# Kernel optimization log

Measured on AMD Instinct MI355X. Metric: run time of the kernel, lower is better.

Reference implementation:

```python
import jax, jax.numpy as jnp
import numpy as np

HEAD_SIZE = 64
N_EMBD = 1024
BLOCK_SIZE = 2048


def setup_inputs() -> dict:
    key = jax.random.key(0)
    ks = jax.random.split(key, 7)
    B, T = 4, 2048
    s = 1.0 / np.sqrt(N_EMBD)
    return {
        "x": jax.random.normal(ks[0], (B, T, N_EMBD), dtype=jnp.float32),
        "Wq": jax.random.normal(ks[1], (N_EMBD, HEAD_SIZE), dtype=jnp.float32) * s,
        "bq": jnp.zeros((HEAD_SIZE,), dtype=jnp.float32),
        "Wk": jax.random.normal(ks[2], (N_EMBD, HEAD_SIZE), dtype=jnp.float32) * s,
        "bk": jnp.zeros((HEAD_SIZE,), dtype=jnp.float32),
        "Wv": jax.random.normal(ks[3], (N_EMBD, HEAD_SIZE), dtype=jnp.float32) * s,
        "bv": jnp.zeros((HEAD_SIZE,), dtype=jnp.float32),
    }


def reference(x, Wq, bq, Wk, bk, Wv, bv):
    # x: [B, T, n_embd]
    B, T, _ = x.shape
    q = x @ Wq + bq  # [B, T, H]
    k = x @ Wk + bk
    v = x @ Wv + bv
    # Faithful to source: divides by head_size**(-0.5) == multiplies by sqrt(head_size)
    scale = jnp.float32(HEAD_SIZE) ** 0.5
    scores = jnp.einsum("bqh,bkh->bqk", q, k) * scale  # [B, T, T]
    causal = jnp.tril(jnp.ones((T, T), dtype=bool))
    scores = jnp.where(causal, scores, -jnp.inf)
    attn = jax.nn.softmax(scores, axis=-1)  # dropout p=0.0 (eval)
    out = jnp.einsum("bqk,bkh->bqh", attn, v)  # [B, T, H]
    return out
```

## Files before the change

### kernel.cpp

```cpp
#include <hip/hip_runtime.h>
#include <math.h>

#define NE 1024
#define HS 64
#define TT 2048
#define QSC 11.541560327111707f

typedef __bf16    v8bf __attribute__((ext_vector_type(8)));
typedef _Float16  v8h  __attribute__((ext_vector_type(8)));
typedef float     v4f  __attribute__((ext_vector_type(4)));

#define MFMA_BF(a, b, c)  __builtin_amdgcn_mfma_f32_16x16x32_bf16((a), (b), (c), 0, 0, 0)
#define MFMA_F16(a, b, c) __builtin_amdgcn_mfma_f32_16x16x32_f16((a), (b), (c), 0, 0, 0)

__device__ __forceinline__ void gl_lds16(const void* g, void* l) {
    __builtin_amdgcn_global_load_lds(
        (const __attribute__((address_space(1))) unsigned int*)g,
        (__attribute__((address_space(3))) unsigned int*)l, 16, 0, 0);
}

#define SYNC_VM(imm) do {                                   \
    __asm__ __volatile__("" ::: "memory");                  \
    __builtin_amdgcn_s_waitcnt(imm);                        \
    __builtin_amdgcn_s_barrier();                           \
    __asm__ __volatile__("" ::: "memory");                  \
} while (0)
#define WAIT_VM4  0x0F74
#define WAIT_VM0  0x0F70

__global__ __launch_bounds__(256) void prep_w(
    const float* __restrict__ Wq, const float* __restrict__ Wk,
    const float* __restrict__ Wv, char* __restrict__ imgW)
{
    __shared__ float t[64][65];
    const int bx = blockIdx.x, by = blockIdx.y;
    const float* W = (by == 0) ? Wq : ((by == 1) ? Wk : Wv);
    const int tid = threadIdx.x;
    const int cc = tid & 63, r4 = tid >> 6;
    #pragma unroll
    for (int p = 0; p < 16; ++p) {
        const int k = p * 4 + r4;
        t[k][cc] = W[(size_t)(bx * 64 + k) * HS + cc];
    }
    __syncthreads();
    #pragma unroll
    for (int e = 0; e < 4; ++e) {
        const int chunk = tid + e * 256;
        const int s2   = chunk >> 9;
        const int rem  = chunk & 511;
        const int ctl  = rem >> 7;
        const int rem2 = rem & 127;
        const int pl   = rem2 >> 6;
        const int rem3 = rem2 & 63;
        const int c    = rem3 >> 2;
        const int p16  = rem3 & 3;
        const int kb   = s2 * 32 + ((p16 ^ (c & 3)) << 3);
        const int ncol = ctl * 16 + c;
        v8bf o;
        #pragma unroll
        for (int j = 0; j < 8; ++j) {
            const float v = t[kb + j][ncol];
            const __bf16 h = (__bf16)v;
            o[j] = pl ? (__bf16)(v - (float)h) : h;
        }
        *(v8bf*)(imgW + (size_t)(bx * 2 + s2) * 24576
                 + (by * 4 + ctl) * 2048 + pl * 1024 + c * 64 + p16 * 16) = o;
    }
}

__global__ __launch_bounds__(256, 2) void proj(
    const float* __restrict__ x, const char* __restrict__ imgW,
    const float* __restrict__ bq, const float* __restrict__ bk,
    const float* __restrict__ bv,
    _Float16* __restrict__ qh, _Float16* __restrict__ ql,
    _Float16* __restrict__ kp, _Float16* __restrict__ vp)
{
    __shared__ __align__(16) char sbuf[3][16384];

    const int tid = threadIdx.x, lane = tid & 63, cg = tid >> 6;
    const int quad = lane >> 4, l16 = lane & 15;
    const int bx = blockIdx.x;
    const int m0 = (bx >> 1) * 32;
    const int h  = bx & 1;

    const int xrow = cg * 8 + (lane >> 3);
    const int xp   = (lane >> 1) & 3;
    const int xh   = lane & 1;
    const float* gx = x + (size_t)(m0 + xrow) * NE
                        + ((xp ^ (xrow & 3)) << 3) + (xh << 2);
    const int xl = cg * 1024 + lane * 16;
    const char* gw = imgW + (size_t)h * 12288 + (size_t)tid * 16;

    v4f acc[3];
    #pragma unroll
    for (int i = 0; i < 3; ++i) acc[i] = (v4f){0.f, 0.f, 0.f, 0.f};

    #define STAGE(ks, xb_)  do {                                          \
        gl_lds16(gx + (ks) * 32, (xb_) + xl);                             \
        const char* gws_ = gw + (size_t)(ks) * 24576;                     \
        _Pragma("unroll")                                                 \
        for (int j_ = 0; j_ < 3; ++j_)                                    \
            gl_lds16(gws_ + j_ * 4096, (xb_) + 4096 + tid * 16 + j_ * 4096); \
    } while (0)

    auto compute = [&](int ks) {
        const char* xb = sbuf[ks % 3];
        const char* wb = xb + 4096;
        const int mt = cg >> 1;
        const int wc = cg & 1;
        const int rl = mt * 16 + l16;
        const int pA = quad ^ (rl & 3);
        const float4 a0 = *(const float4*)(xb + rl * 128 + pA * 32);
        const float4 a1 = *(const float4*)(xb + rl * 128 + pA * 32 + 16);
        const float av[8] = {a0.x, a0.y, a0.z, a0.w, a1.x, a1.y, a1.z, a1.w};
        v8bf ah, al;
        #pragma unroll
        for (int i = 0; i < 8; ++i) {
            const __bf16 hv = (__bf16)av[i];
            ah[i] = hv;
            al[i] = (__bf16)(av[i] - (float)hv);
        }
        const int wo = l16 * 64 + ((quad ^ (l16 & 3)) << 4);
        #pragma unroll
        for (int j = 0; j < 3; ++j) {
            const char* base = wb + (wc * 3 + j) * 2048 + wo;
            const v8bf bh = *(const v8bf*)(base);
            const v8bf bl = *(const v8bf*)(base + 1024);
            acc[j] = MFMA_BF(ah, bh, acc[j]);
            acc[j] = MFMA_BF(ah, bl, acc[j]);
            acc[j] = MFMA_BF(al, bh, acc[j]);
        }
    };

    STAGE(0, sbuf[0]);
    STAGE(1, sbuf[1]);
    for (int ks = 0; ks < 31; ++ks) {
        SYNC_VM(WAIT_VM4);
        if (ks + 2 < 32) STAGE(ks + 2, sbuf[(ks + 2) % 3]);
        compute(ks);
    }
    SYNC_VM(WAIT_VM0);
    compute(31);
    #undef STAGE

    const int mt = cg >> 1, wc = cg & 1;
    #pragma unroll
    for (int j = 0; j < 3; ++j) {
        const int n = h * 96 + wc * 48 + j * 16 + l16;
        const float bias = (n < 64) ? bq[n] : ((n < 128) ? bk[n - 64] : bv[n - 128]);
        #pragma unroll
        for (int reg = 0; reg < 4; ++reg) {
            const int row = m0 + mt * 16 + quad * 4 + reg;
            const float v = acc[j][reg] + bias;
            if (n < 64) {
                const float s = v * QSC;
                const _Float16 hh = (_Float16)s;
                qh[(size_t)row * HS + n] = hh;
                ql[(size_t)row * HS + n] = (_Float16)(s - (float)hh);
            } else if (n < 128) {
                const int b2 = row >> 11, t = row & 2047, hc = n - 64;
                const size_t base = ((size_t)(b2 * 128) + (t >> 4)) * 1024;
                const int off = (hc < 32)
                    ? (hc >> 3) * 128 + (t & 15) * 8 + (hc & 7)
                    : 512 + ((hc - 32) >> 3) * 128 + (t & 15) * 8 + (hc & 7);
                kp[base + off] = (_Float16)v;
            } else {
                const int b2 = row >> 11, t = row & 2047, hc = n - 128;
                const int cj = t >> 6, tp = t & 63, hg = hc >> 4, hr = hc & 15;
                const size_t base = (((size_t)(b2 * 32) + cj) * 4 + hg) * 1024;
                const int off = (tp < 32)
                    ? (tp >> 3) * 128 + hr * 8 + (tp & 7)
                    : 512 + ((tp - 32) >> 3) * 128 + hr * 8 + (tp & 7);
                vp[base + off] = (_Float16)v;
            }
        }
    }
}

__global__ __launch_bounds__(512, 2) void attn(
    const _Float16* __restrict__ qh, const _Float16* __restrict__ ql,
    const _Float16* __restrict__ kp, const _Float16* __restrict__ vp,
    float* __restrict__ out)
{
    __shared__ __align__(16) char smem_raw[69632];
    _Float16* ps = (_Float16*)smem_raw;
    float*    os = (float*)smem_raw;
    __shared__ float sm[8][2][16], sl[8][2][16];

    const int tid = threadIdx.x, lane = tid & 63, w = tid >> 6;
    const int quad = lane >> 4, l16 = lane & 15;
    const int b = blockIdx.x & 3, pair = blockIdx.x >> 2;
    const int q0t[2] = {(127 - pair) * 16, pair * 16};
    const int ntk0 = (q0t[0] + 16 + 63) >> 6;
    const int ntk1 = (q0t[1] + 16 + 63) >> 6;
    const int total = ntk0 + ntk1;

    v8h Qh0[2], Qh1[2], Ql0[2], Ql1[2];
    #pragma unroll
    for (int t = 0; t < 2; ++t) {
        const size_t qrow = ((size_t)b * TT + q0t[t] + l16) * HS;
        Qh0[t] = *(const v8h*)(qh + qrow + quad * 8);
        Qh1[t] = *(const v8h*)(qh + qrow + 32 + quad * 8);
        Ql0[t] = *(const v8h*)(ql + qrow + quad * 8);
        Ql1[t] = *(const v8h*)(ql + qrow + 32 + quad * 8);
    }

    const v8h vones = {(_Float16)1.f, (_Float16)1.f, (_Float16)1.f, (_Float16)1.f,
                       (_Float16)1.f, (_Float16)1.f, (_Float16)1.f, (_Float16)1.f};

    float mr0[4] = {-3e38f, -3e38f, -3e38f, -3e38f};
    float mr1[4] = {-3e38f, -3e38f, -3e38f, -3e38f};
    v4f o0[4], o1[4], l40, l41;
    #pragma unroll
    for (int i = 0; i < 4; ++i) {
        o0[i] = (v4f){0.f, 0.f, 0.f, 0.f};
        o1[i] = (v4f){0.f, 0.f, 0.f, 0.f};
    }
    l40 = (v4f){0.f, 0.f, 0.f, 0.f};
    l41 = (v4f){0.f, 0.f, 0.f, 0.f};

    _Float16* pw = ps + w * (16 * 72);

    auto loadK = [&](int j0, v8h (&Kf)[8]) {
        #pragma unroll
        for (int nt = 0; nt < 4; ++nt) {
            const _Float16* kb = kp + ((size_t)(b * 128) + (j0 >> 4) + nt) * 1024
                                    + lane * 8;
            Kf[nt * 2]     = *(const v8h*)(kb);
            Kf[nt * 2 + 1] = *(const v8h*)(kb + 512);
        }
    };

    auto doChunk = [&](int j0, int q0c, int t, const v8h (&Kf)[8],
                       float (&mrow)[4], v4f (&o)[4], v4f &o4) {
        v8h Vf[8];
        #pragma unroll
        for (int nt = 0; nt < 4; ++nt) {
            const _Float16* vb = vp + (((size_t)(b * 32) + (j0 >> 6)) * 4 + nt) * 1024
                                    + lane * 8;
            Vf[nt * 2]     = *(const v8h*)(vb);
            Vf[nt * 2 + 1] = *(const v8h*)(vb + 512);
        }
        v4f s[4];
        #pragma unroll
        for (int i = 0; i < 4; ++i) s[i] = (v4f){0.f, 0.f, 0.f, 0.f};
        #pragma unroll
        for (int nt = 0; nt < 4; ++nt) {
            s[nt] = MFMA_F16(Qh0[t], Kf[nt * 2],     s[nt]);
            s[nt] = MFMA_F16(Qh1[t], Kf[nt * 2 + 1], s[nt]);
            s[nt] = MFMA_F16(Ql0[t], Kf[nt * 2],     s[nt]);
            s[nt] = MFMA_F16(Ql1[t], Kf[nt * 2 + 1], s[nt]);
        }
        const int irow = q0c + quad * 4;
        float mx[4] = {-3e38f, -3e38f, -3e38f, -3e38f};
        #pragma unroll
        for (int nt = 0; nt < 4; ++nt)
            #pragma unroll
            for (int reg = 0; reg < 4; ++reg) {
                if (j0 + nt * 16 + l16 > irow + reg) s[nt][reg] = -3e38f;
                mx[reg] = fmaxf(mx[reg], s[nt][reg]);
            }
        #pragma unroll
        for (int off = 8; off; off >>= 1)
            #pragma unroll
            for (int reg = 0; reg < 4; ++reg)
                mx[reg] = fmaxf(mx[reg], __shfl_xor(mx[reg], off));
        float al[4];
        #pragma unroll
        for (int reg = 0; reg < 4; ++reg) {
            const float mn = fmaxf(mrow[reg], mx[reg]);
            al[reg] = exp2f(mrow[reg] - mn);
            mrow[reg] = mn;
        }
        #pragma unroll
        for (int nt = 0; nt < 4; ++nt)
            #pragma unroll
            for (int reg = 0; reg < 4; ++reg) {
                const float p = (j0 + nt * 16 + l16 > irow + reg)
                                    ? 0.f : exp2f(s[nt][reg] - mrow[reg]);
                pw[(quad * 4 + reg) * 72 + nt * 16 + l16] = (_Float16)p;
            }
        #pragma unroll
        for (int nt = 0; nt < 4; ++nt)
            #pragma unroll
            for (int reg = 0; reg < 4; ++reg)
                o[nt][reg] *= al[reg];
        #pragma unroll
        for (int reg = 0; reg < 4; ++reg)
            o4[reg] *= al[reg];
        const v8h Pa0 = *(const v8h*)(pw + l16 * 72 + quad * 8);
        const v8h Pa1 = *(const v8h*)(pw + l16 * 72 + 32 + quad * 8);
        #pragma unroll
        for (int nt = 0; nt < 4; ++nt) {
            o[nt] = MFMA_F16(Pa0, Vf[nt * 2],     o[nt]);
            o[nt] = MFMA_F16(Pa1, Vf[nt * 2 + 1], o[nt]);
        }
        o4 = MFMA_F16(Pa0, vones, o4);
        o4 = MFMA_F16(Pa1, vones, o4);
    };

    auto jof = [&](int c) { return (c < ntk0) ? c * 64 : (c - ntk0) * 64; };

    {
        v8h KA[8], KB[8];
        int c = w;
        loadK(jof(c), KA);
        while (true) {
            int cn = c + 8;
            if (cn < total) loadK(jof(cn), KB);
            if (c < ntk0) doChunk(c * 64,          q0t[0], 0, KA, mr0, o0, l40);
            else          doChunk((c - ntk0) * 64, q0t[1], 1, KA, mr1, o1, l41);
            if (cn >= total) break;
            c = cn; cn = c + 8;
            if (cn < total) loadK(jof(cn), KA);
            if (c < ntk0) doChunk(c * 64,          q0t[0], 0, KB, mr0, o0, l40);
            else          doChunk((c - ntk0) * 64, q0t[1], 1, KB, mr1, o1, l41);
            if (cn >= total) break;
            c = cn;
        }
    }

    if (l16 == 0) {
        #pragma unroll
        for (int reg = 0; reg < 4; ++reg) {
            sm[w][0][quad * 4 + reg] = mr0[reg];
            sl[w][0][quad * 4 + reg] = l40[reg];
            sm[w][1][quad * 4 + reg] = mr1[reg];
            sl[w][1][quad * 4 + reg] = l41[reg];
        }
    }
    __syncthreads();

    #pragma unroll
    for (int t = 0; t < 2; ++t) {
        float sc[4];
        #pragma unroll
        for (int reg = 0; reg < 4; ++reg) {
            const int r = quad * 4 + reg;
            float M = sm[0][t][r];
            #pragma unroll
            for (int i = 1; i < 8; ++i) M = fmaxf(M, sm[i][t][r]);
            const float mw = t ? mr1[reg] : mr0[reg];
            sc[reg] = exp2f(mw - M);
        }
        float* ow = os + (size_t)(w * 2 + t) * (16 * 68);
        #pragma unroll
        for (int nt = 0; nt < 4; ++nt)
            #pragma unroll
            for (int reg = 0; reg < 4; ++reg) {
                const v4f& oo = t ? o1[nt] : o0[nt];
                ow[(quad * 4 + reg) * 68 + nt * 16 + l16] = oo[reg] * sc[reg];
            }
    }
    __syncthreads();

    #pragma unroll
    for (int kk = 0; kk < 4; ++kk) {
        const int g = w * 4 + kk;
        const int t = g >> 4, m = g & 15;
        float M = sm[0][t][m];
        #pragma unroll
        for (int i = 1; i < 8; ++i) M = fmaxf(M, sm[i][t][m]);
        float L = 0.f, val = 0.f;
        #pragma unroll
        for (int i = 0; i < 8; ++i) {
            L   += sl[i][t][m] * exp2f(sm[i][t][m] - M);
            val += os[(size_t)(i * 2 + t) * (16 * 68) + m * 68 + lane];
        }
        out[((size_t)b * TT + q0t[t] + m) * HS + lane] = val / L;
    }
}

extern "C" void kernel_launch(void* const* d_in, const int* in_sizes, int n_in,
                              void* d_out, int out_size, void* d_ws, size_t ws_size,
                              hipStream_t stream)
{
    const float* x  = (const float*)d_in[0];
    const float* Wq = (const float*)d_in[1];
    const float* bq = (const float*)d_in[2];
    const float* Wk = (const float*)d_in[3];
    const float* bk = (const float*)d_in[4];
    const float* Wv = (const float*)d_in[5];
    const float* bv = (const float*)d_in[6];
    float* out = (float*)d_out;

    const int rows = in_sizes[0] / NE;
    char* p = (char*)d_ws;
    char* imgW = p;                           p += (size_t)32 * 24576;
    _Float16* qhb = (_Float16*)p;             p += (size_t)rows * HS * 2;
    _Float16* qlb = (_Float16*)p;             p += (size_t)rows * HS * 2;
    _Float16* kpb = (_Float16*)p;             p += (size_t)rows * HS * 2;
    _Float16* vpb = (_Float16*)p;             p += (size_t)rows * HS * 2;

    prep_w<<<dim3(16, 3), 256, 0, stream>>>(Wq, Wk, Wv, imgW);
    proj<<<rows / 16, 256, 0, stream>>>(x, imgW, bq, bk, bv,
                                        qhb, qlb, kpb, vpb);
    attn<<<rows / 32, 512, 0, stream>>>(qhb, qlb, kpb, vpb, out);
}
```

Measured before the change: 122.1 us.

## Assign one 16-row query tile per block instead of paired causal tiles

```diff
diff --git a/kernel.cpp b/kernel.cpp
--- a/kernel.cpp
+++ b/kernel.cpp
@@ -182,42 +182,35 @@
     const _Float16* __restrict__ kp, const _Float16* __restrict__ vp,
     float* __restrict__ out)
 {
-    __shared__ __align__(16) char smem_raw[69632];
+    __shared__ __align__(16) char smem_raw[57344];
     _Float16* ps = (_Float16*)smem_raw;
     float*    os = (float*)smem_raw;
-    __shared__ float sm[8][2][16], sl[8][2][16];
+    __shared__ float sm[8][16], sl[8][16];
 
     const int tid = threadIdx.x, lane = tid & 63, w = tid >> 6;
     const int quad = lane >> 4, l16 = lane & 15;
-    const int b = blockIdx.x & 3, pair = blockIdx.x >> 2;
-    const int q0t[2] = {(127 - pair) * 16, pair * 16};
-    const int ntk0 = (q0t[0] + 16 + 63) >> 6;
-    const int ntk1 = (q0t[1] + 16 + 63) >> 6;
-    const int total = ntk0 + ntk1;
-
-    v8h Qh0[2], Qh1[2], Ql0[2], Ql1[2];
-    #pragma unroll
-    for (int t = 0; t < 2; ++t) {
-        const size_t qrow = ((size_t)b * TT + q0t[t] + l16) * HS;
-        Qh0[t] = *(const v8h*)(qh + qrow + quad * 8);
-        Qh1[t] = *(const v8h*)(qh + qrow + 32 + quad * 8);
-        Ql0[t] = *(const v8h*)(ql + qrow + quad * 8);
-        Ql1[t] = *(const v8h*)(ql + qrow + 32 + quad * 8);
+    const int bx = blockIdx.x;
+    const int b = bx & 3, tile = 127 - (bx >> 2);
+    const int q0 = tile * 16;
+    const int ntk = (q0 + 16 + 63) >> 6;
+
+    v8h Qh0, Qh1, Ql0, Ql1;
+    {
+        const size_t qrow = ((size_t)b * TT + q0 + l16) * HS;
+        Qh0 = *(const v8h*)(qh + qrow + quad * 8);
+        Qh1 = *(const v8h*)(qh + qrow + 32 + quad * 8);
+        Ql0 = *(const v8h*)(ql + qrow + quad * 8);
+        Ql1 = *(const v8h*)(ql + qrow + 32 + quad * 8);
     }
 
     const v8h vones = {(_Float16)1.f, (_Float16)1.f, (_Float16)1.f, (_Float16)1.f,
                        (_Float16)1.f, (_Float16)1.f, (_Float16)1.f, (_Float16)1.f};
 
-    float mr0[4] = {-3e38f, -3e38f, -3e38f, -3e38f};
-    float mr1[4] = {-3e38f, -3e38f, -3e38f, -3e38f};
-    v4f o0[4], o1[4], l40, l41;
-    #pragma unroll
-    for (int i = 0; i < 4; ++i) {
-        o0[i] = (v4f){0.f, 0.f, 0.f, 0.f};
-        o1[i] = (v4f){0.f, 0.f, 0.f, 0.f};
-    }
-    l40 = (v4f){0.f, 0.f, 0.f, 0.f};
-    l41 = (v4f){0.f, 0.f, 0.f, 0.f};
+    float mr[4] = {-3e38f, -3e38f, -3e38f, -3e38f};
+    v4f o[4], l4;
+    #pragma unroll
+    for (int i = 0; i < 4; ++i) o[i] = (v4f){0.f, 0.f, 0.f, 0.f};
+    l4 = (v4f){0.f, 0.f, 0.f, 0.f};
 
     _Float16* pw = ps + w * (16 * 72);
 
@@ -231,8 +224,7 @@
         }
     };
 
-    auto doChunk = [&](int j0, int q0c, int t, const v8h (&Kf)[8],
-                       float (&mrow)[4], v4f (&o)[4], v4f &o4) {
+    auto doChunk = [&](int j0, const v8h (&Kf)[8]) {
         v8h Vf[8];
         #pragma unroll
         for (int nt = 0; nt < 4; ++nt) {
@@ -246,12 +238,12 @@
         for (int i = 0; i < 4; ++i) s[i] = (v4f){0.f, 0.f, 0.f, 0.f};
         #pragma unroll
         for (int nt = 0; nt < 4; ++nt) {
-            s[nt] = MFMA_F16(Qh0[t], Kf[nt * 2],     s[nt]);
-            s[nt] = MFMA_F16(Qh1[t], Kf[nt * 2 + 1], s[nt]);
-            s[nt] = MFMA_F16(Ql0[t], Kf[nt * 2],     s[nt]);
-            s[nt] = MFMA_F16(Ql1[t], Kf[nt * 2 + 1], s[nt]);
-        }
-        const int irow = q0c + quad * 4;
+            s[nt] = MFMA_F16(Qh0, Kf[nt * 2],     s[nt]);
+            s[nt] = MFMA_F16(Qh1, Kf[nt * 2 + 1], s[nt]);
+            s[nt] = MFMA_F16(Ql0, Kf[nt * 2],     s[nt]);
+            s[nt] = MFMA_F16(Ql1, Kf[nt * 2 + 1], s[nt]);
+        }
+        const int irow = q0 + quad * 4;
         float mx[4] = {-3e38f, -3e38f, -3e38f, -3e38f};
         #pragma unroll
         for (int nt = 0; nt < 4; ++nt)
@@ -268,16 +260,16 @@
         float al[4];
         #pragma unroll
         for (int reg = 0; reg < 4; ++reg) {
-            const float mn = fmaxf(mrow[reg], mx[reg]);
-            al[reg] = exp2f(mrow[reg] - mn);
-            mrow[reg] = mn;
+            const float mn = fmaxf(mr[reg], mx[reg]);
+            al[reg] = exp2f(mr[reg] - mn);
+            mr[reg] = mn;
         }
         #pragma unroll
         for (int nt = 0; nt < 4; ++nt)
             #pragma unroll
             for (int reg = 0; reg < 4; ++reg) {
                 const float p = (j0 + nt * 16 + l16 > irow + reg)
-                                    ? 0.f : exp2f(s[nt][reg] - mrow[reg]);
+                                    ? 0.f : exp2f(s[nt][reg] - mr[reg]);
                 pw[(quad * 4 + reg) * 72 + nt * 16 + l16] = (_Float16)p;
             }
         #pragma unroll
@@ -287,7 +279,7 @@
                 o[nt][reg] *= al[reg];
         #pragma unroll
         for (int reg = 0; reg < 4; ++reg)
-            o4[reg] *= al[reg];
+            l4[reg] *= al[reg];
         const v8h Pa0 = *(const v8h*)(pw + l16 * 72 + quad * 8);
         const v8h Pa1 = *(const v8h*)(pw + l16 * 72 + 32 + quad * 8);
         #pragma unroll
@@ -295,27 +287,23 @@
             o[nt] = MFMA_F16(Pa0, Vf[nt * 2],     o[nt]);
             o[nt] = MFMA_F16(Pa1, Vf[nt * 2 + 1], o[nt]);
         }
-        o4 = MFMA_F16(Pa0, vones, o4);
-        o4 = MFMA_F16(Pa1, vones, o4);
+        l4 = MFMA_F16(Pa0, vones, l4);
+        l4 = MFMA_F16(Pa1, vones, l4);
     };
 
-    auto jof = [&](int c) { return (c < ntk0) ? c * 64 : (c - ntk0) * 64; };
-
-    {
+    if (w < ntk) {
         v8h KA[8], KB[8];
         int c = w;
-        loadK(jof(c), KA);
+        loadK(c * 64, KA);
         while (true) {
             int cn = c + 8;
-            if (cn < total) loadK(jof(cn), KB);
-            if (c < ntk0) doChunk(c * 64,          q0t[0], 0, KA, mr0, o0, l40);
-            else          doChunk((c - ntk0) * 64, q0t[1], 1, KA, mr1, o1, l41);
-            if (cn >= total) break;
+            if (cn < ntk) loadK(cn * 64, KB);
+            doChunk(c * 64, KA);
+            if (cn >= ntk) break;
             c = cn; cn = c + 8;
-            if (cn < total) loadK(jof(cn), KA);
-            if (c < ntk0) doChunk(c * 64,          q0t[0], 0, KB, mr0, o0, l40);
-            else          doChunk((c - ntk0) * 64, q0t[1], 1, KB, mr1, o1, l41);
-            if (cn >= total) break;
+            if (cn < ntk) loadK(cn * 64, KA);
+            doChunk(c * 64, KB);
+            if (cn >= ntk) break;
             c = cn;
         }
     }
@@ -323,51 +311,44 @@
     if (l16 == 0) {
         #pragma unroll
         for (int reg = 0; reg < 4; ++reg) {
-            sm[w][0][quad * 4 + reg] = mr0[reg];
-            sl[w][0][quad * 4 + reg] = l40[reg];
-            sm[w][1][quad * 4 + reg] = mr1[reg];
-            sl[w][1][quad * 4 + reg] = l41[reg];
+            sm[w][quad * 4 + reg] = mr[reg];
+            sl[w][quad * 4 + reg] = l4[reg];
         }
     }
     __syncthreads();
 
-    #pragma unroll
-    for (int t = 0; t < 2; ++t) {
+    {
         float sc[4];
         #pragma unroll
         for (int reg = 0; reg < 4; ++reg) {
             const int r = quad * 4 + reg;
-            float M = sm[0][t][r];
-            #pragma unroll
-            for (int i = 1; i < 8; ++i) M = fmaxf(M, sm[i][t][r]);
-            const float mw = t ? mr1[reg] : mr0[reg];
-            sc[reg] = exp2f(mw - M);
-        }
-        float* ow = os + (size_t)(w * 2 + t) * (16 * 68);
+            float M = sm[0][r];
+            #pragma unroll
+            for (int i = 1; i < 8; ++i) M = fmaxf(M, sm[i][r]);
+            sc[reg] = exp2f(mr[reg] - M);
+        }
+        float* ow = os + (size_t)w * (16 * 68);
         #pragma unroll
         for (int nt = 0; nt < 4; ++nt)
             #pragma unroll
-            for (int reg = 0; reg < 4; ++reg) {
-                const v4f& oo = t ? o1[nt] : o0[nt];
-                ow[(quad * 4 + reg) * 68 + nt * 16 + l16] = oo[reg] * sc[reg];
-            }
+            for (int reg = 0; reg < 4; ++reg)
+                ow[(quad * 4 + reg) * 68 + nt * 16 + l16] = o[nt][reg] * sc[reg];
     }
     __syncthreads();
 
     #pragma unroll
-    for (int kk = 0; kk < 4; ++kk) {
-        const int g = w * 4 + kk;
-        const int t = g >> 4, m = g & 15;
-        float M = sm[0][t][m];
-        #pragma unroll
-        for (int i = 1; i < 8; ++i) M = fmaxf(M, sm[i][t][m]);
+    for (int kk = 0; kk < 2; ++kk) {
+        const int m = w * 2 + kk;
+        float M = sm[0][m];
+        #pragma unroll
+        for (int i = 1; i < 8; ++i) M = fmaxf(M, sm[i][m]);
         float L = 0.f, val = 0.f;
         #pragma unroll
         for (int i = 0; i < 8; ++i) {
-            L   += sl[i][t][m] * exp2f(sm[i][t][m] - M);
-            val += os[(size_t)(i * 2 + t) * (16 * 68) + m * 68 + lane];
-        }
-        out[((size_t)b * TT + q0t[t] + m) * HS + lane] = val / L;
+            L   += sl[i][m] * exp2f(sm[i][m] - M);
+            val += os[(size_t)i * (16 * 68) + m * 68 + lane];
+        }
+        out[((size_t)b * TT + q0 + m) * HS + lane] = val / L;
     }
 }
 
@@ -395,5 +376,5 @@
     prep_w<<<dim3(16, 3), 256, 0, stream>>>(Wq, Wk, Wv, imgW);
     proj<<<rows / 16, 256, 0, stream>>>(x, imgW, bq, bk, bv,
                                         qhb, qlb, kpb, vpb);
-    attn<<<rows / 32, 512, 0, stream>>>(qhb, qlb, kpb, vpb, out);
-}
+    attn<<<rows / 16, 512, 0, stream>>>(qhb, qlb, kpb, vpb, out);
+}
```

New measurement: 121.5 us. Within noise of the previous version (-0.5%).
